# Kernel tuning notes

Measured on AMD Instinct MI355X. Metric: run time of the kernel, lower is better.

Reference implementation:

```python
import jax, jax.numpy as jnp
import numpy as np

IN = 128      # input_size
HID = 64      # fast_net hidden width
NFW = IN * HID + HID  # 8256 flat fast weights (layer1 then layer2)
B = 256


def setup_inputs() -> dict:
    key = jax.random.key(0)
    k1, k2, k3, k4 = jax.random.split(key, 4)
    x = jax.random.normal(k1, (B, 1, IN), dtype=jnp.float32)
    # updater network weights: Linear(IN, 2*NFW, bias=False) then Linear(2*NFW, NFW, bias=False)
    W1 = jax.random.normal(k2, (2 * NFW, IN), dtype=jnp.float32) * 0.02
    W2 = jax.random.normal(k3, (NFW, 2 * NFW), dtype=jnp.float32) * 0.02
    # initial flat fast weights, in (0,1) since the update squashes there
    fw0 = jax.random.uniform(k4, (NFW,), dtype=jnp.float32)
    return {"x": x, "W1": W1, "W2": W2, "fw0": fw0}


def reference(x, W1, W2, fw0):
    xs = x[:, 0, :]  # [B, IN]
    # updater network has no weight updates itself -> batch the two matmuls
    U = (xs @ W1.T) @ W2.T  # [B, NFW] per-sample weight updates
    gain, shift = jnp.float32(10.0), jnp.float32(0.5)

    def step(fw, inp):
        x_i, u_i = inp
        # update_func: 1 / (1 + exp(-10*(w + u - 0.5)))
        fw = jax.nn.sigmoid(gain * (fw + u_i - shift))
        w1 = fw[: IN * HID].reshape(HID, IN)   # fast layer 1 [HID, IN]
        w2 = fw[IN * HID:].reshape(1, HID)     # fast layer 2 [1, HID]
        pred = w2 @ jax.nn.relu(w1 @ x_i)      # [1]
        return fw, pred

    _, preds = jax.lax.scan(step, fw0, (xs, U))  # sequential over batch, state persists
    return preds  # [B, 1]
```

## Files before the change

kernel.cpp:

```cpp
#include <hip/hip_runtime.h>
#include <hip/hip_bf16.h>

#define IN_DIM 128
#define HID    64
#define NFW    8256
#define BATCH  256
#define K2     16512
#define BM     64
#define NMB    129
#define KSPLIT 6
#define NT_PER 43
#define GRID_M 774

typedef float f32x4 __attribute__((ext_vector_type(4)));
typedef short bf16x8 __attribute__((ext_vector_type(8)));

__device__ __forceinline__ unsigned int f2bf(float f) {
    union { float f; unsigned int u; } v; v.f = f;
    return (v.u + 0x7FFFu + ((v.u >> 16) & 1u)) >> 16;
}

__global__ __launch_bounds__(256) void k_prep_w1t(const float* __restrict__ W1,
                                                  unsigned short* __restrict__ W1T) {
    __shared__ float tile[64][IN_DIM + 1];
    const int kt = blockIdx.x;
    const int t  = threadIdx.x;
    const float* src = W1 + (size_t)kt * 64 * IN_DIM;
#pragma unroll
    for (int p = 0; p < 8; ++p) {
        int c4 = p * 256 + t;
        int e = c4 * 4;
        int row = e >> 7, col = e & 127;
        f32x4 v = *reinterpret_cast<const f32x4*>(src + row * IN_DIM + col);
        tile[row][col+0] = v.x; tile[row][col+1] = v.y;
        tile[row][col+2] = v.z; tile[row][col+3] = v.w;
    }
    __syncthreads();
    unsigned short* dst = W1T + (size_t)kt * (IN_DIM * 64);
#pragma unroll
    for (int it = 0; it < 4; ++it) {
        int c = it * 256 + t;
        int n = c >> 3, kl0 = (c & 7) * 8;
        uint4 w;
        w.x = f2bf(tile[kl0+0][n]) | (f2bf(tile[kl0+1][n]) << 16);
        w.y = f2bf(tile[kl0+2][n]) | (f2bf(tile[kl0+3][n]) << 16);
        w.z = f2bf(tile[kl0+4][n]) | (f2bf(tile[kl0+5][n]) << 16);
        w.w = f2bf(tile[kl0+6][n]) | (f2bf(tile[kl0+7][n]) << 16);
        *reinterpret_cast<uint4*>(dst + c * 8) = w;
    }
}

__global__ __launch_bounds__(256, 3) void k_gemm_M(const float* __restrict__ W2,
                                                   const unsigned short* __restrict__ W1T,
                                                   float* __restrict__ Mpart) {
    __shared__ __align__(16) unsigned char smem[49152];
    float* trs = reinterpret_cast<float*>(smem);

    const int t = threadIdx.x;
    const int lane = t & 63, wid = t >> 6;
    const int wm = wid >> 1, wn = wid & 1;
    const int l15 = lane & 15, l4 = (lane >> 4) & 3;

    const int b = blockIdx.x;
    const int xcd = b & 7, slot = b >> 3;
    const int p = (xcd < 6) ? (xcd * 97 + slot) : (582 + (xcd - 6) * 96 + slot);
    const int ks = p / NMB, mb = p % NMB;

    const int m0 = mb * BM;
    const int g0 = ks * NT_PER;
    const int kt0 = (p * 7) % NT_PER;

    const int ar  = t >> 2;
    const int ac  = (t & 3) * 16;
    const int asw = (ar & 7) << 4;
    const float* abase = W2 + (size_t)(m0 + ar) * K2 + (size_t)g0 * 64 + ac;
    const int bn  = t >> 1;
    const int bko = (t & 1) * 32;
    const int bsw = (bn & 7) << 4;
    const unsigned short* bbase = W1T + (size_t)g0 * 8192 + bn * 64 + bko;

    f32x4 sa0, sa1, sa2, sa3;
    uint4 sb0, sb1, sb2, sb3;
    f32x4 acc[2][4];
#pragma unroll
    for (int mf = 0; mf < 2; ++mf)
#pragma unroll
        for (int nf = 0; nf < 4; ++nf)
            acc[mf][nf] = (f32x4){0.f, 0.f, 0.f, 0.f};

#define LOADREGS(KT) {                                                         \
    const float* _ap = abase + (size_t)(KT) * 64;                              \
    sa0 = *reinterpret_cast<const f32x4*>(_ap);                                \
    sa1 = *reinterpret_cast<const f32x4*>(_ap + 4);                            \
    sa2 = *reinterpret_cast<const f32x4*>(_ap + 8);                            \
    sa3 = *reinterpret_cast<const f32x4*>(_ap + 12);                           \
    const unsigned short* _bp = bbase + (size_t)(KT) * 8192;                   \
    sb0 = *reinterpret_cast<const uint4*>(_bp);                                \
    sb1 = *reinterpret_cast<const uint4*>(_bp + 8);                            \
    sb2 = *reinterpret_cast<const uint4*>(_bp + 16);                           \
    sb3 = *reinterpret_cast<const uint4*>(_bp + 24); }

#define STOREREGS(BUF) {                                                       \
    unsigned char* _Ash = smem + ((BUF) << 13);                                \
    unsigned char* _Bsh = smem + 16384 + ((BUF) << 14);                        \
    uint4 _w0, _w1;                                                            \
    _w0.x = f2bf(sa0.x) | (f2bf(sa0.y) << 16);                                 \
    _w0.y = f2bf(sa0.z) | (f2bf(sa0.w) << 16);                                 \
    _w0.z = f2bf(sa1.x) | (f2bf(sa1.y) << 16);                                 \
    _w0.w = f2bf(sa1.z) | (f2bf(sa1.w) << 16);                                 \
    _w1.x = f2bf(sa2.x) | (f2bf(sa2.y) << 16);                                 \
    _w1.y = f2bf(sa2.z) | (f2bf(sa2.w) << 16);                                 \
    _w1.z = f2bf(sa3.x) | (f2bf(sa3.y) << 16);                                 \
    _w1.w = f2bf(sa3.z) | (f2bf(sa3.w) << 16);                                 \
    const int _ab = (t & 3) * 32;                                              \
    *reinterpret_cast<uint4*>(&_Ash[ar * 128 + ((_ab)      ^ asw)]) = _w0;     \
    *reinterpret_cast<uint4*>(&_Ash[ar * 128 + ((_ab + 16) ^ asw)]) = _w1;     \
    const int _bb = (t & 1) * 64;                                              \
    *reinterpret_cast<uint4*>(&_Bsh[bn * 128 + ((_bb)      ^ bsw)]) = sb0;     \
    *reinterpret_cast<uint4*>(&_Bsh[bn * 128 + ((_bb + 16) ^ bsw)]) = sb1;     \
    *reinterpret_cast<uint4*>(&_Bsh[bn * 128 + ((_bb + 32) ^ bsw)]) = sb2;     \
    *reinterpret_cast<uint4*>(&_Bsh[bn * 128 + ((_bb + 48) ^ bsw)]) = sb3; }

#define MFMA_PHASE(BUF) {                                                      \
    const unsigned char* _Ash = smem + ((BUF) << 13);                          \
    const unsigned char* _Bsh = smem + 16384 + ((BUF) << 14);                  \
    _Pragma("unroll")                                                          \
    for (int kk = 0; kk < 2; ++kk) {                                           \
        _Pragma("unroll")                                                      \
        for (int mf = 0; mf < 2; ++mf) {                                       \
            const int arow = wm * 32 + mf * 16 + l15;                          \
            bf16x8 af = *reinterpret_cast<const bf16x8*>(                      \
                &_Ash[arow * 128 + ((kk * 64 + l4 * 16) ^ ((arow & 7) << 4))]);\
            _Pragma("unroll")                                                  \
            for (int nf = 0; nf < 4; ++nf) {                                   \
                const int brow = wn * 64 + nf * 16 + l15;                      \
                bf16x8 bfr = *reinterpret_cast<const bf16x8*>(                 \
                    &_Bsh[brow * 128 + ((kk * 64 + l4 * 16) ^ ((brow & 7) << 4))]); \
                acc[mf][nf] = __builtin_amdgcn_mfma_f32_16x16x32_bf16(         \
                    af, bfr, acc[mf][nf], 0, 0, 0);                            \
            }                                                                  \
        }                                                                      \
    } }

#define LBAR() { asm volatile("s_waitcnt lgkmcnt(0)" ::: "memory");            \
                 __builtin_amdgcn_s_barrier();                                 \
                 __builtin_amdgcn_sched_barrier(0); }

    int kreg = kt0;
    LOADREGS(kreg);
    STOREREGS(0);
    { int kn = kreg + 1; if (kn >= NT_PER) kn = 0; kreg = kn; }
    LOADREGS(kreg);
    LBAR();

    int cur = 0;
#pragma unroll 1
    for (int i = 0; i < NT_PER; ++i) {
        if (i + 1 < NT_PER) {
            STOREREGS(cur ^ 1);
        }
        if (i + 2 < NT_PER) {
            int kn = kreg + 1; if (kn >= NT_PER) kn = 0; kreg = kn;
            LOADREGS(kreg);
        }
        MFMA_PHASE(cur);
        LBAR();
        cur ^= 1;
    }

    float* outp = Mpart + (size_t)ks * ((size_t)NFW * IN_DIM) + (size_t)m0 * IN_DIM;
#pragma unroll 1
    for (int w = 0; w < 2; ++w) {
        __syncthreads();
        if (wm == w) {
#pragma unroll
            for (int mf = 0; mf < 2; ++mf)
#pragma unroll
                for (int nf = 0; nf < 4; ++nf)
#pragma unroll
                    for (int r = 0; r < 4; ++r)
                        trs[(mf * 16 + l4 * 4 + r) * 132 + wn * 64 + nf * 16 + l15] = acc[mf][nf][r];
        }
        __syncthreads();
#pragma unroll
        for (int q = 0; q < 4; ++q) {
            int idx = q * 256 + t;
            int rr = idx >> 5, c4 = (idx & 31) << 2;
            f32x4 v = *reinterpret_cast<const f32x4*>(&trs[rr * 132 + c4]);
            *reinterpret_cast<f32x4*>(outp + (size_t)(w * 32 + rr) * IN_DIM + c4) = v;
        }
    }
#undef LOADREGS
#undef STOREREGS
#undef MFMA_PHASE
#undef LBAR
}

__global__ __launch_bounds__(256) void k_reduce_M(const float* __restrict__ Mpart,
                                                  unsigned short* __restrict__ Mb) {
    const int idx = blockIdx.x * 256 + threadIdx.x;
    f32x4 s = (f32x4){0.f, 0.f, 0.f, 0.f};
#pragma unroll
    for (int ks = 0; ks < KSPLIT; ++ks) {
        f32x4 v = *reinterpret_cast<const f32x4*>(
            Mpart + (size_t)ks * ((size_t)NFW * IN_DIM) + (size_t)idx * 4);
        s.x += v.x; s.y += v.y; s.z += v.z; s.w += v.w;
    }
    uint2 o;
    o.x = f2bf(s.x) | (f2bf(s.y) << 16);
    o.y = f2bf(s.z) | (f2bf(s.w) << 16);
    *reinterpret_cast<uint2*>(Mb + (size_t)idx * 4) = o;
}

__global__ __launch_bounds__(256) void k_gemm_U(const float* __restrict__ xs,
                                                const unsigned short* __restrict__ Mb,
                                                float* __restrict__ U) {
    const int t = threadIdx.x, lane = t & 63, wid = t >> 6;
    const int l15 = lane & 15, l4 = lane >> 4;
    const int bj = blockIdx.x % 129, bi = blockIdx.x / 129;
    const int i0 = bi * 64 + wid * 16;
    const int j0 = bj * 64;
    f32x4 acc[4];
#pragma unroll
    for (int nf = 0; nf < 4; ++nf) acc[nf] = (f32x4){0.f, 0.f, 0.f, 0.f};
#pragma unroll
    for (int kk = 0; kk < 4; ++kk) {
        const float* xp = xs + (size_t)(i0 + l15) * IN_DIM + kk * 32 + l4 * 8;
        f32x4 x0 = *reinterpret_cast<const f32x4*>(xp);
        f32x4 x1 = *reinterpret_cast<const f32x4*>(xp + 4);
        union { bf16x8 v; unsigned short s[8]; } af;
        af.s[0] = f2bf(x0.x); af.s[1] = f2bf(x0.y);
        af.s[2] = f2bf(x0.z); af.s[3] = f2bf(x0.w);
        af.s[4] = f2bf(x1.x); af.s[5] = f2bf(x1.y);
        af.s[6] = f2bf(x1.z); af.s[7] = f2bf(x1.w);
#pragma unroll
        for (int nf = 0; nf < 4; ++nf) {
            const unsigned short* mp = Mb + (size_t)(j0 + nf * 16 + l15) * IN_DIM + kk * 32 + l4 * 8;
            bf16x8 bfr = *reinterpret_cast<const bf16x8*>(mp);
            acc[nf] = __builtin_amdgcn_mfma_f32_16x16x32_bf16(af.v, bfr, acc[nf], 0, 0, 0);
        }
    }
    const int iw = i0 + l4 * 4;
#pragma unroll
    for (int nf = 0; nf < 4; ++nf) {
        const int j = j0 + nf * 16 + l15;
#pragma unroll
        for (int r = 0; r < 4; ++r)
            U[(size_t)(iw + r) * NFW + j] = acc[nf][r];
    }
}

__global__ __launch_bounds__(64) void k_chains(const float* __restrict__ U,
                                               const float* __restrict__ fw0,
                                               float* __restrict__ FW) {
    const int j = blockIdx.x * 64 + threadIdx.x;
    float fw = fw0[j];
    const float* up = U + j;
    float* fp = FW + j;
    float ucur[16], unxt[16];
#pragma unroll
    for (int q = 0; q < 16; ++q) ucur[q] = up[(size_t)q * NFW];
    for (int ib = 0; ib < BATCH; ib += 16) {
        if (ib + 16 < BATCH) {
#pragma unroll
            for (int q = 0; q < 16; ++q) unxt[q] = up[(size_t)(ib + 16 + q) * NFW];
        }
#pragma unroll
        for (int q = 0; q < 16; ++q) {
            float z = 10.0f * (fw + ucur[q] - 0.5f);
            fw = 1.0f / (1.0f + __expf(-z));
            fp[(size_t)(ib + q) * NFW] = fw;
        }
#pragma unroll
        for (int q = 0; q < 16; ++q) ucur[q] = unxt[q];
    }
}

__global__ __launch_bounds__(256) void k_preds(const float* __restrict__ FW,
                                               const float* __restrict__ xs,
                                               float* __restrict__ out) {
    __shared__ float xsh[IN_DIM];
    __shared__ float hsh[HID];
    const int i = blockIdx.x, t = threadIdx.x;
    if (t < 32) {
        f32x4 v = *reinterpret_cast<const f32x4*>(xs + (size_t)i * IN_DIM + t * 4);
        xsh[t*4+0] = v.x; xsh[t*4+1] = v.y; xsh[t*4+2] = v.z; xsh[t*4+3] = v.w;
    }
    __syncthreads();
    const int k = t >> 2, q = t & 3;
    const float* fr = FW + (size_t)i * NFW + k * IN_DIM + q * 32;
    float p = 0.f;
#pragma unroll
    for (int m = 0; m < 8; ++m) {
        f32x4 v = *reinterpret_cast<const f32x4*>(fr + m * 4);
        const int d = q * 32 + m * 4;
        p += v.x * xsh[d] + v.y * xsh[d+1] + v.z * xsh[d+2] + v.w * xsh[d+3];
    }
    p += __shfl_xor(p, 1);
    p += __shfl_xor(p, 2);
    if (q == 0) hsh[k] = fmaxf(p, 0.f);
    __syncthreads();
    if (t < 64) {
        float v = FW[(size_t)i * NFW + IN_DIM * HID + t] * hsh[t];
        v += __shfl_xor(v, 1);  v += __shfl_xor(v, 2);  v += __shfl_xor(v, 4);
        v += __shfl_xor(v, 8);  v += __shfl_xor(v, 16); v += __shfl_xor(v, 32);
        if (t == 0) out[i] = v;
    }
}

extern "C" void kernel_launch(void* const* d_in, const int* in_sizes, int n_in,
                              void* d_out, int out_size, void* d_ws, size_t ws_size,
                              hipStream_t stream) {
    const float* x   = (const float*)d_in[0];
    const float* W1  = (const float*)d_in[1];
    const float* W2  = (const float*)d_in[2];
    const float* fw0 = (const float*)d_in[3];
    float* out = (float*)d_out;

    char* ws = (char*)d_ws;
    unsigned short* W1T   = (unsigned short*)(ws);
    float*          Mpart = (float*)(ws + 4227072);
    unsigned short* Mb    = (unsigned short*)(ws + 29589504);
    float*          U     = (float*)(ws + 31703040);
    float*          FW    = (float*)(ws + 40157184);

    hipLaunchKernelGGL(k_prep_w1t, dim3(258),    dim3(256), 0, stream, W1, W1T);
    hipLaunchKernelGGL(k_gemm_M,   dim3(GRID_M), dim3(256), 0, stream, W2, W1T, Mpart);
    hipLaunchKernelGGL(k_reduce_M, dim3(1032),   dim3(256), 0, stream, Mpart, Mb);
    hipLaunchKernelGGL(k_gemm_U,   dim3(516),    dim3(256), 0, stream, x, Mb, U);
    hipLaunchKernelGGL(k_chains,   dim3(129),    dim3(64),  0, stream, U, fw0, FW);
    hipLaunchKernelGGL(k_preds,    dim3(256),    dim3(256), 0, stream, FW, x, out);
}
```

Measured before the change: 200.6 us.

## Enlarge M-GEMM tile to 96 rows and fuse U GEMM into chain kernel

The W2·W1 GEMM now uses 96-row tiles with three MFMA row fragments per wave. This cuts the grid to 516 blocks at two blocks per CU, giving more reuse of each B tile at the cost of more LDS and registers. Separately, the U=x·M GEMM and the sequential sigmoid chains are fused into one kernel: each block computes its 256×64 U slice into LDS, then one wave runs the recurrence from LDS. This removes the U global round-trip and one launch, but the chain step now uses only 129 waves, with three of the four waves per block idle during it.

```diff
diff --git a/kernel.cpp b/kernel.cpp
--- a/kernel.cpp
+++ b/kernel.cpp
@@ -6,11 +6,11 @@
 #define NFW    8256
 #define BATCH  256
 #define K2     16512
-#define BM     64
-#define NMB    129
+#define BM     96
+#define NMB    86
 #define KSPLIT 6
 #define NT_PER 43
-#define GRID_M 774
+#define GRID_M 516
 
 typedef float f32x4 __attribute__((ext_vector_type(4)));
 typedef short bf16x8 __attribute__((ext_vector_type(8)));
@@ -50,10 +50,10 @@
     }
 }
 
-__global__ __launch_bounds__(256, 3) void k_gemm_M(const float* __restrict__ W2,
+__global__ __launch_bounds__(256, 2) void k_gemm_M(const float* __restrict__ W2,
                                                    const unsigned short* __restrict__ W1T,
                                                    float* __restrict__ Mpart) {
-    __shared__ __align__(16) unsigned char smem[49152];
+    __shared__ __align__(16) unsigned char smem[57344];
     float* trs = reinterpret_cast<float*>(smem);
 
     const int t = threadIdx.x;
@@ -63,27 +63,26 @@
 
     const int b = blockIdx.x;
     const int xcd = b & 7, slot = b >> 3;
-    const int p = (xcd < 6) ? (xcd * 97 + slot) : (582 + (xcd - 6) * 96 + slot);
+    const int p = (xcd < 4) ? (xcd * 65 + slot) : (260 + (xcd - 4) * 64 + slot);
     const int ks = p / NMB, mb = p % NMB;
 
     const int m0 = mb * BM;
     const int g0 = ks * NT_PER;
     const int kt0 = (p * 7) % NT_PER;
 
-    const int ar  = t >> 2;
-    const int ac  = (t & 3) * 16;
+    const int ar  = t >> 3;
+    const int ac  = (t & 7) * 8;
     const int asw = (ar & 7) << 4;
     const float* abase = W2 + (size_t)(m0 + ar) * K2 + (size_t)g0 * 64 + ac;
     const int bn  = t >> 1;
-    const int bko = (t & 1) * 32;
     const int bsw = (bn & 7) << 4;
-    const unsigned short* bbase = W1T + (size_t)g0 * 8192 + bn * 64 + bko;
-
-    f32x4 sa0, sa1, sa2, sa3;
+    const unsigned short* bbase = W1T + (size_t)g0 * 8192 + bn * 64 + (t & 1) * 32;
+
+    f32x4 sa0, sa1, sa2, sa3, sa4, sa5;
     uint4 sb0, sb1, sb2, sb3;
-    f32x4 acc[2][4];
-#pragma unroll
-    for (int mf = 0; mf < 2; ++mf)
+    f32x4 acc[3][4];
+#pragma unroll
+    for (int mf = 0; mf < 3; ++mf)
 #pragma unroll
         for (int nf = 0; nf < 4; ++nf)
             acc[mf][nf] = (f32x4){0.f, 0.f, 0.f, 0.f};
@@ -92,29 +91,32 @@
     const float* _ap = abase + (size_t)(KT) * 64;                              \
     sa0 = *reinterpret_cast<const f32x4*>(_ap);                                \
     sa1 = *reinterpret_cast<const f32x4*>(_ap + 4);                            \
-    sa2 = *reinterpret_cast<const f32x4*>(_ap + 8);                            \
-    sa3 = *reinterpret_cast<const f32x4*>(_ap + 12);                           \
+    sa2 = *reinterpret_cast<const f32x4*>(_ap + (size_t)32 * K2);              \
+    sa3 = *reinterpret_cast<const f32x4*>(_ap + (size_t)32 * K2 + 4);          \
+    sa4 = *reinterpret_cast<const f32x4*>(_ap + (size_t)64 * K2);              \
+    sa5 = *reinterpret_cast<const f32x4*>(_ap + (size_t)64 * K2 + 4);          \
     const unsigned short* _bp = bbase + (size_t)(KT) * 8192;                   \
     sb0 = *reinterpret_cast<const uint4*>(_bp);                                \
     sb1 = *reinterpret_cast<const uint4*>(_bp + 8);                            \
     sb2 = *reinterpret_cast<const uint4*>(_bp + 16);                           \
     sb3 = *reinterpret_cast<const uint4*>(_bp + 24); }
 
+#define CVT16(W, LO, HI) { W.x = f2bf(LO.x) | (f2bf(LO.y) << 16);              \
+                           W.y = f2bf(LO.z) | (f2bf(LO.w) << 16);              \
+                           W.z = f2bf(HI.x) | (f2bf(HI.y) << 16);              \
+                           W.w = f2bf(HI.z) | (f2bf(HI.w) << 16); }
+
 #define STOREREGS(BUF) {                                                       \
-    unsigned char* _Ash = smem + ((BUF) << 13);                                \
-    unsigned char* _Bsh = smem + 16384 + ((BUF) << 14);                        \
-    uint4 _w0, _w1;                                                            \
-    _w0.x = f2bf(sa0.x) | (f2bf(sa0.y) << 16);                                 \
-    _w0.y = f2bf(sa0.z) | (f2bf(sa0.w) << 16);                                 \
-    _w0.z = f2bf(sa1.x) | (f2bf(sa1.y) << 16);                                 \
-    _w0.w = f2bf(sa1.z) | (f2bf(sa1.w) << 16);                                 \
-    _w1.x = f2bf(sa2.x) | (f2bf(sa2.y) << 16);                                 \
-    _w1.y = f2bf(sa2.z) | (f2bf(sa2.w) << 16);                                 \
-    _w1.z = f2bf(sa3.x) | (f2bf(sa3.y) << 16);                                 \
-    _w1.w = f2bf(sa3.z) | (f2bf(sa3.w) << 16);                                 \
-    const int _ab = (t & 3) * 32;                                              \
-    *reinterpret_cast<uint4*>(&_Ash[ar * 128 + ((_ab)      ^ asw)]) = _w0;     \
-    *reinterpret_cast<uint4*>(&_Ash[ar * 128 + ((_ab + 16) ^ asw)]) = _w1;     \
+    unsigned char* _Ash = smem + (BUF) * 12288;                                \
+    unsigned char* _Bsh = smem + 24576 + (BUF) * 16384;                        \
+    uint4 _w;                                                                  \
+    const int _abyte = (t & 7) * 16;                                           \
+    CVT16(_w, sa0, sa1);                                                       \
+    *reinterpret_cast<uint4*>(&_Ash[(ar)      * 128 + (_abyte ^ asw)]) = _w;   \
+    CVT16(_w, sa2, sa3);                                                       \
+    *reinterpret_cast<uint4*>(&_Ash[(ar + 32) * 128 + (_abyte ^ asw)]) = _w;   \
+    CVT16(_w, sa4, sa5);                                                       \
+    *reinterpret_cast<uint4*>(&_Ash[(ar + 64) * 128 + (_abyte ^ asw)]) = _w;   \
     const int _bb = (t & 1) * 64;                                              \
     *reinterpret_cast<uint4*>(&_Bsh[bn * 128 + ((_bb)      ^ bsw)]) = sb0;     \
     *reinterpret_cast<uint4*>(&_Bsh[bn * 128 + ((_bb + 16) ^ bsw)]) = sb1;     \
@@ -122,24 +124,38 @@
     *reinterpret_cast<uint4*>(&_Bsh[bn * 128 + ((_bb + 48) ^ bsw)]) = sb3; }
 
 #define MFMA_PHASE(BUF) {                                                      \
-    const unsigned char* _Ash = smem + ((BUF) << 13);                          \
-    const unsigned char* _Bsh = smem + 16384 + ((BUF) << 14);                  \
+    const unsigned char* _Ash = smem + (BUF) * 12288;                          \
+    const unsigned char* _Bsh = smem + 24576 + (BUF) * 16384;                  \
+    const int _fsw = (l15 & 7) << 4;                                           \
     _Pragma("unroll")                                                          \
     for (int kk = 0; kk < 2; ++kk) {                                           \
-        _Pragma("unroll")                                                      \
-        for (int mf = 0; mf < 2; ++mf) {                                       \
-            const int arow = wm * 32 + mf * 16 + l15;                          \
-            bf16x8 af = *reinterpret_cast<const bf16x8*>(                      \
-                &_Ash[arow * 128 + ((kk * 64 + l4 * 16) ^ ((arow & 7) << 4))]);\
-            _Pragma("unroll")                                                  \
-            for (int nf = 0; nf < 4; ++nf) {                                   \
-                const int brow = wn * 64 + nf * 16 + l15;                      \
-                bf16x8 bfr = *reinterpret_cast<const bf16x8*>(                 \
-                    &_Bsh[brow * 128 + ((kk * 64 + l4 * 16) ^ ((brow & 7) << 4))]); \
-                acc[mf][nf] = __builtin_amdgcn_mfma_f32_16x16x32_bf16(         \
-                    af, bfr, acc[mf][nf], 0, 0, 0);                            \
-            }                                                                  \
-        }                                                                      \
+        const int _fc = (kk * 64 + l4 * 16) ^ _fsw;                            \
+        bf16x8 af0 = *reinterpret_cast<const bf16x8*>(                         \
+            &_Ash[(wm * 48 +  0 + l15) * 128 + _fc]);                          \
+        bf16x8 af1 = *reinterpret_cast<const bf16x8*>(                         \
+            &_Ash[(wm * 48 + 16 + l15) * 128 + _fc]);                          \
+        bf16x8 af2 = *reinterpret_cast<const bf16x8*>(                         \
+            &_Ash[(wm * 48 + 32 + l15) * 128 + _fc]);                          \
+        bf16x8 bf0 = *reinterpret_cast<const bf16x8*>(                         \
+            &_Bsh[(wn * 64 +  0 + l15) * 128 + _fc]);                          \
+        bf16x8 bf1 = *reinterpret_cast<const bf16x8*>(                         \
+            &_Bsh[(wn * 64 + 16 + l15) * 128 + _fc]);                          \
+        bf16x8 bf2 = *reinterpret_cast<const bf16x8*>(                         \
+            &_Bsh[(wn * 64 + 32 + l15) * 128 + _fc]);                          \
+        bf16x8 bf3 = *reinterpret_cast<const bf16x8*>(                         \
+            &_Bsh[(wn * 64 + 48 + l15) * 128 + _fc]);                          \
+        acc[0][0] = __builtin_amdgcn_mfma_f32_16x16x32_bf16(af0, bf0, acc[0][0], 0, 0, 0); \
+        acc[0][1] = __builtin_amdgcn_mfma_f32_16x16x32_bf16(af0, bf1, acc[0][1], 0, 0, 0); \
+        acc[0][2] = __builtin_amdgcn_mfma_f32_16x16x32_bf16(af0, bf2, acc[0][2], 0, 0, 0); \
+        acc[0][3] = __builtin_amdgcn_mfma_f32_16x16x32_bf16(af0, bf3, acc[0][3], 0, 0, 0); \
+        acc[1][0] = __builtin_amdgcn_mfma_f32_16x16x32_bf16(af1, bf0, acc[1][0], 0, 0, 0); \
+        acc[1][1] = __builtin_amdgcn_mfma_f32_16x16x32_bf16(af1, bf1, acc[1][1], 0, 0, 0); \
+        acc[1][2] = __builtin_amdgcn_mfma_f32_16x16x32_bf16(af1, bf2, acc[1][2], 0, 0, 0); \
+        acc[1][3] = __builtin_amdgcn_mfma_f32_16x16x32_bf16(af1, bf3, acc[1][3], 0, 0, 0); \
+        acc[2][0] = __builtin_amdgcn_mfma_f32_16x16x32_bf16(af2, bf0, acc[2][0], 0, 0, 0); \
+        acc[2][1] = __builtin_amdgcn_mfma_f32_16x16x32_bf16(af2, bf1, acc[2][1], 0, 0, 0); \
+        acc[2][2] = __builtin_amdgcn_mfma_f32_16x16x32_bf16(af2, bf2, acc[2][2], 0, 0, 0); \
+        acc[2][3] = __builtin_amdgcn_mfma_f32_16x16x32_bf16(af2, bf3, acc[2][3], 0, 0, 0); \
     } }
 
 #define LBAR() { asm volatile("s_waitcnt lgkmcnt(0)" ::: "memory");            \
@@ -174,7 +190,7 @@
         __syncthreads();
         if (wm == w) {
 #pragma unroll
-            for (int mf = 0; mf < 2; ++mf)
+            for (int mf = 0; mf < 3; ++mf)
 #pragma unroll
                 for (int nf = 0; nf < 4; ++nf)
 #pragma unroll
@@ -183,14 +199,15 @@
         }
         __syncthreads();
 #pragma unroll
-        for (int q = 0; q < 4; ++q) {
+        for (int q = 0; q < 6; ++q) {
             int idx = q * 256 + t;
             int rr = idx >> 5, c4 = (idx & 31) << 2;
             f32x4 v = *reinterpret_cast<const f32x4*>(&trs[rr * 132 + c4]);
-            *reinterpret_cast<f32x4*>(outp + (size_t)(w * 32 + rr) * IN_DIM + c4) = v;
+            *reinterpret_cast<f32x4*>(outp + (size_t)(w * 48 + rr) * IN_DIM + c4) = v;
         }
     }
 #undef LOADREGS
+#undef CVT16
 #undef STOREREGS
 #undef MFMA_PHASE
 #undef LBAR
@@ -212,67 +229,62 @@
     *reinterpret_cast<uint2*>(Mb + (size_t)idx * 4) = o;
 }
 
-__global__ __launch_bounds__(256) void k_gemm_U(const float* __restrict__ xs,
-                                                const unsigned short* __restrict__ Mb,
-                                                float* __restrict__ U) {
+__global__ __launch_bounds__(256) void k_uchains(const float* __restrict__ xs,
+                                                 const unsigned short* __restrict__ Mb,
+                                                 const float* __restrict__ fw0,
+                                                 float* __restrict__ FW) {
+    __shared__ float Ulds[256][68];
     const int t = threadIdx.x, lane = t & 63, wid = t >> 6;
-    const int l15 = lane & 15, l4 = lane >> 4;
-    const int bj = blockIdx.x % 129, bi = blockIdx.x / 129;
-    const int i0 = bi * 64 + wid * 16;
-    const int j0 = bj * 64;
-    f32x4 acc[4];
-#pragma unroll
-    for (int nf = 0; nf < 4; ++nf) acc[nf] = (f32x4){0.f, 0.f, 0.f, 0.f};
-#pragma unroll
-    for (int kk = 0; kk < 4; ++kk) {
-        const float* xp = xs + (size_t)(i0 + l15) * IN_DIM + kk * 32 + l4 * 8;
-        f32x4 x0 = *reinterpret_cast<const f32x4*>(xp);
-        f32x4 x1 = *reinterpret_cast<const f32x4*>(xp + 4);
-        union { bf16x8 v; unsigned short s[8]; } af;
-        af.s[0] = f2bf(x0.x); af.s[1] = f2bf(x0.y);
-        af.s[2] = f2bf(x0.z); af.s[3] = f2bf(x0.w);
-        af.s[4] = f2bf(x1.x); af.s[5] = f2bf(x1.y);
-        af.s[6] = f2bf(x1.z); af.s[7] = f2bf(x1.w);
-#pragma unroll
-        for (int nf = 0; nf < 4; ++nf) {
-            const unsigned short* mp = Mb + (size_t)(j0 + nf * 16 + l15) * IN_DIM + kk * 32 + l4 * 8;
-            bf16x8 bfr = *reinterpret_cast<const bf16x8*>(mp);
-            acc[nf] = __builtin_amdgcn_mfma_f32_16x16x32_bf16(af.v, bfr, acc[nf], 0, 0, 0);
-        }
-    }
-    const int iw = i0 + l4 * 4;
-#pragma unroll
-    for (int nf = 0; nf < 4; ++nf) {
-        const int j = j0 + nf * 16 + l15;
-#pragma unroll
-        for (int r = 0; r < 4; ++r)
-            U[(size_t)(iw + r) * NFW + j] = acc[nf][r];
-    }
-}
-
-__global__ __launch_bounds__(64) void k_chains(const float* __restrict__ U,
-                                               const float* __restrict__ fw0,
-                                               float* __restrict__ FW) {
-    const int j = blockIdx.x * 64 + threadIdx.x;
-    float fw = fw0[j];
-    const float* up = U + j;
-    float* fp = FW + j;
-    float ucur[16], unxt[16];
-#pragma unroll
-    for (int q = 0; q < 16; ++q) ucur[q] = up[(size_t)q * NFW];
-    for (int ib = 0; ib < BATCH; ib += 16) {
-        if (ib + 16 < BATCH) {
-#pragma unroll
-            for (int q = 0; q < 16; ++q) unxt[q] = up[(size_t)(ib + 16 + q) * NFW];
-        }
-#pragma unroll
-        for (int q = 0; q < 16; ++q) {
-            float z = 10.0f * (fw + ucur[q] - 0.5f);
+    const int l15 = lane & 15, l4 = (lane >> 4) & 3;
+    const int j0 = blockIdx.x * 64;
+
+    bf16x8 bfr[4][4];
+#pragma unroll
+    for (int kk = 0; kk < 4; ++kk)
+#pragma unroll
+        for (int nf = 0; nf < 4; ++nf)
+            bfr[kk][nf] = *reinterpret_cast<const bf16x8*>(
+                Mb + (size_t)(j0 + nf * 16 + l15) * IN_DIM + kk * 32 + l4 * 8);
+
+#pragma unroll 1
+    for (int ib = 0; ib < 4; ++ib) {
+        const int i0 = wid * 64 + ib * 16;
+        f32x4 acc[4];
+#pragma unroll
+        for (int nf = 0; nf < 4; ++nf) acc[nf] = (f32x4){0.f, 0.f, 0.f, 0.f};
+#pragma unroll
+        for (int kk = 0; kk < 4; ++kk) {
+            const float* xp = xs + (size_t)(i0 + l15) * IN_DIM + kk * 32 + l4 * 8;
+            f32x4 x0 = *reinterpret_cast<const f32x4*>(xp);
+            f32x4 x1 = *reinterpret_cast<const f32x4*>(xp + 4);
+            union { bf16x8 v; unsigned short s[8]; } af;
+            af.s[0] = f2bf(x0.x); af.s[1] = f2bf(x0.y);
+            af.s[2] = f2bf(x0.z); af.s[3] = f2bf(x0.w);
+            af.s[4] = f2bf(x1.x); af.s[5] = f2bf(x1.y);
+            af.s[6] = f2bf(x1.z); af.s[7] = f2bf(x1.w);
+#pragma unroll
+            for (int nf = 0; nf < 4; ++nf)
+                acc[nf] = __builtin_amdgcn_mfma_f32_16x16x32_bf16(af.v, bfr[kk][nf], acc[nf], 0, 0, 0);
+        }
+#pragma unroll
+        for (int nf = 0; nf < 4; ++nf)
+#pragma unroll
+            for (int r = 0; r < 4; ++r)
+                Ulds[i0 + l4 * 4 + r][nf * 16 + l15] = acc[nf][r];
+    }
+    __syncthreads();
+
+    if (wid == 0) {
+        const int j = j0 + lane;
+        float fw = fw0[j];
+        float* fp = FW + j;
+#pragma unroll 8
+        for (int i = 0; i < BATCH; ++i) {
+            float u = Ulds[i][lane];
+            float z = 10.0f * (fw + u - 0.5f);
             fw = 1.0f / (1.0f + __expf(-z));
-            fp[(size_t)(ib + q) * NFW] = fw;
-        }
-#pragma unroll
-        for (int q = 0; q < 16; ++q) ucur[q] = unxt[q];
+            fp[(size_t)i * NFW] = fw;
+        }
     }
 }
 
@@ -321,13 +333,11 @@
     unsigned short* W1T   = (unsigned short*)(ws);
     float*          Mpart = (float*)(ws + 4227072);
     unsigned short* Mb    = (unsigned short*)(ws + 29589504);
-    float*          U     = (float*)(ws + 31703040);
-    float*          FW    = (float*)(ws + 40157184);
+    float*          FW    = (float*)(ws + 31703040);
 
     hipLaunchKernelGGL(k_prep_w1t, dim3(258),    dim3(256), 0, stream, W1, W1T);
     hipLaunchKernelGGL(k_gemm_M,   dim3(GRID_M), dim3(256), 0, stream, W2, W1T, Mpart);
     hipLaunchKernelGGL(k_reduce_M, dim3(1032),   dim3(256), 0, stream, Mpart, Mb);
-    hipLaunchKernelGGL(k_gemm_U,   dim3(516),    dim3(256), 0, stream, x, Mb, U);
-    hipLaunchKernelGGL(k_chains,   dim3(129),    dim3(64),  0, stream, U, fw0, FW);
+    hipLaunchKernelGGL(k_uchains,  dim3(129),    dim3(256), 0, stream, x, Mb, fw0, FW);
     hipLaunchKernelGGL(k_preds,    dim3(256),    dim3(256), 0, stream, FW, x, out);
 }
```

Result: faster. 184.9 us (-7.8%).
